# Kernel optimization log

Measured on AMD Instinct MI355X. Metric: run time of the kernel, lower is better.

The kernel has to match this reference:

```python
import jax, jax.numpy as jnp
import numpy as np

OUT = 50  # out_shape


def setup_inputs() -> dict:
    key = jax.random.key(0)
    k1, k2 = jax.random.split(key)
    B, C, H, W, N = 8, 3, 1024, 1024, 128
    x = jax.random.normal(k1, (B, C, H, W), dtype=jnp.float32)
    u = jax.random.uniform(k2, (N, 4), dtype=jnp.float32)
    # valid normalized cxcywh boxes (fully in-bounds, non-degenerate)
    cx = 0.3 + 0.4 * u[:, 0]
    cy = 0.3 + 0.4 * u[:, 1]
    w = 0.1 + 0.2 * u[:, 2]
    h = 0.1 + 0.2 * u[:, 3]
    bbox = jnp.stack([cx, cy, w, h], axis=-1)
    return {"x": x, "bbox": bbox}


def _xyxy_int(bbox, H, W):
    # its_denormalize_time: normalized cxcywh -> pixel cxcywh; its_xyxy_time: -> int xyxy
    scale = jnp.array([W, H, W, H], dtype=jnp.float32)
    b = bbox * scale
    cx, cy, w, h = b[:, 0], b[:, 1], b[:, 2], b[:, 3]
    x1 = jnp.clip(jnp.floor(cx - w / 2).astype(jnp.int32), 0, W - 1)
    y1 = jnp.clip(jnp.floor(cy - h / 2).astype(jnp.int32), 0, H - 1)
    x2 = jnp.clip(jnp.floor(cx + w / 2).astype(jnp.int32), 0, W)
    y2 = jnp.clip(jnp.floor(cy + h / 2).astype(jnp.int32), 0, H)
    x2 = jnp.maximum(x2, x1 + 1)
    y2 = jnp.maximum(y2, y1 + 1)
    return x1, y1, x2, y2


def _src_coords(lo, hi):
    # torch bilinear (align_corners=False) sampling coords inside crop [lo, hi)
    n = (hi - lo).astype(jnp.float32)
    s = jnp.clip((jnp.arange(OUT, dtype=jnp.float32) + 0.5) * n / OUT - 0.5, 0.0, n - 1.0)
    i0 = jnp.floor(s)
    w1 = s - i0
    i0 = i0.astype(jnp.int32)
    i1 = jnp.minimum(i0 + 1, hi - lo - 1)
    return lo + i0, lo + i1, w1  # absolute indices + lerp weight


def _crop_resize(x, x1, y1, x2, y2):
    # fused gather + bilinear resize for one box: [B,C,H,W] -> [B,C,OUT,OUT]
    gy0, gy1, wy = _src_coords(y1, y2)
    gx0, gx1, wx = _src_coords(x1, x2)
    v00 = x[:, :, gy0[:, None], gx0[None, :]]
    v01 = x[:, :, gy0[:, None], gx1[None, :]]
    v10 = x[:, :, gy1[:, None], gx0[None, :]]
    v11 = x[:, :, gy1[:, None], gx1[None, :]]
    top = (1.0 - wx) * v00 + wx * v01
    bot = (1.0 - wx) * v10 + wx * v11
    return (1.0 - wy)[:, None] * top + wy[:, None] * bot


def reference(x, bbox):
    B, C, H, W = x.shape
    x1, y1, x2, y2 = _xyxy_int(bbox, H, W)
    # vmap over the N boxes -> [N, B, C, OUT, OUT] (stacked version of the list)
    return jax.vmap(lambda a, b, c, d: _crop_resize(x, a, b, c, d))(x1, y1, x2, y2)
```

## Files before the change

kernel.cpp:

```cpp
#include <hip/hip_runtime.h>
#include <hip/hip_bf16.h>

#define OUTN 50
constexpr int B_ = 8, C_ = 3, H_ = 1024, W_ = 1024, N_ = 128;

__global__ __launch_bounds__(256) void crop_resize_kernel(
    const float* __restrict__ x,
    const float* __restrict__ bbox,
    float* __restrict__ out)
{
    const int blk = blockIdx.x;
    const int n  = blk / (B_ * C_);
    const int bc = blk % (B_ * C_);

    __shared__ int   sgy0[OUTN], sgy1[OUTN], sgx0[OUTN], sgx1[OUTN];
    __shared__ float swy[OUTN], swx[OUTN];

    const int t = threadIdx.x;

    if (t < 2 * OUTN) {
        const float cx = bbox[n * 4 + 0] * (float)W_;
        const float cy = bbox[n * 4 + 1] * (float)H_;
        const float bw = bbox[n * 4 + 2] * (float)W_;
        const float bh = bbox[n * 4 + 3] * (float)H_;

        int x1 = min(max((int)floorf(cx - bw / 2.0f), 0), W_ - 1);
        int y1 = min(max((int)floorf(cy - bh / 2.0f), 0), H_ - 1);
        int x2 = min(max((int)floorf(cx + bw / 2.0f), 0), W_);
        int y2 = min(max((int)floorf(cy + bh / 2.0f), 0), H_);
        x2 = max(x2, x1 + 1);
        y2 = max(y2, y1 + 1);

        const bool isY = (t >= OUTN);
        const int  i   = isY ? (t - OUTN) : t;
        const int  lo  = isY ? y1 : x1;
        const int  hi  = isY ? y2 : x2;

        const float nn = (float)(hi - lo);
        float s = ((float)i + 0.5f) * nn / 50.0f - 0.5f;
        s = fminf(fmaxf(s, 0.0f), nn - 1.0f);
        const float i0f = floorf(s);
        const float w1  = s - i0f;
        const int i0 = (int)i0f;
        const int i1 = min(i0 + 1, hi - lo - 1);

        if (isY) { sgy0[i] = lo + i0; sgy1[i] = lo + i1; swy[i] = w1; }
        else     { sgx0[i] = lo + i0; sgx1[i] = lo + i1; swx[i] = w1; }
    }
    __syncthreads();

    const float* __restrict__ xp = x + (size_t)bc * (H_ * W_);
    float* __restrict__ op = out + ((size_t)n * (B_ * C_) + bc) * (OUTN * OUTN);

    for (int idx = t; idx < OUTN * OUTN; idx += blockDim.x) {
        const int oy = idx / OUTN;
        const int ox = idx - oy * OUTN;

        const int gy0 = sgy0[oy], gy1 = sgy1[oy];
        const int gx0 = sgx0[ox], gx1 = sgx1[ox];
        const float wy = swy[oy], wx = swx[ox];

        const float v00 = xp[(size_t)gy0 * W_ + gx0];
        const float v01 = xp[(size_t)gy0 * W_ + gx1];
        const float v10 = xp[(size_t)gy1 * W_ + gx0];
        const float v11 = xp[(size_t)gy1 * W_ + gx1];

        const float top = (1.0f - wx) * v00 + wx * v01;
        const float bot = (1.0f - wx) * v10 + wx * v11;
        op[idx] = (1.0f - wy) * top + wy * bot;
    }
}

extern "C" void kernel_launch(void* const* d_in, const int* in_sizes, int n_in,
                              void* d_out, int out_size, void* d_ws, size_t ws_size,
                              hipStream_t stream) {
    const float* x    = (const float*)d_in[0];
    const float* bbox = (const float*)d_in[1];
    float* out = (float*)d_out;

    const int nblocks = N_ * B_ * C_;
    crop_resize_kernel<<<nblocks, 256, 0, stream>>>(x, bbox, out);
}
```

Measured before the change: 158.8 us.

## Remap blocks per XCD, pair bilinear taps into float2 loads, nontemporal stores

```diff
diff --git a/kernel.cpp b/kernel.cpp
--- a/kernel.cpp
+++ b/kernel.cpp
@@ -3,26 +3,32 @@
 
 #define OUTN 50
 constexpr int B_ = 8, C_ = 3, H_ = 1024, W_ = 1024, N_ = 128;
+constexpr int PLANES = B_ * C_;
+constexpr int PIX    = OUTN * OUTN;
+constexpr int TPB    = 256;
+constexpr int ITER   = (PIX + TPB - 1) / TPB;
 
-__global__ __launch_bounds__(256) void crop_resize_kernel(
+__global__ __launch_bounds__(TPB) void crop_resize_kernel(
     const float* __restrict__ x,
     const float* __restrict__ bbox,
     float* __restrict__ out)
 {
     const int blk = blockIdx.x;
-    const int n  = blk / (B_ * C_);
-    const int bc = blk % (B_ * C_);
+    const int xcd = blk & 7;
+    const int r   = blk >> 3;
+    const int bc  = xcd * 3 + (r % 3);
+    const int n   = r / 3;
 
-    __shared__ int   sgy0[OUTN], sgy1[OUTN], sgx0[OUTN], sgx1[OUTN];
-    __shared__ float swy[OUTN], swx[OUTN];
+    __shared__ int4 sy[OUTN], sx[OUTN];
 
     const int t = threadIdx.x;
 
     if (t < 2 * OUTN) {
-        const float cx = bbox[n * 4 + 0] * (float)W_;
-        const float cy = bbox[n * 4 + 1] * (float)H_;
-        const float bw = bbox[n * 4 + 2] * (float)W_;
-        const float bh = bbox[n * 4 + 3] * (float)H_;
+        const float4 bb = reinterpret_cast<const float4*>(bbox)[n];
+        const float cx = bb.x * (float)W_;
+        const float cy = bb.y * (float)H_;
+        const float bw = bb.z * (float)W_;
+        const float bh = bb.w * (float)H_;
 
         int x1 = min(max((int)floorf(cx - bw / 2.0f), 0), W_ - 1);
         int y1 = min(max((int)floorf(cy - bh / 2.0f), 0), H_ - 1);
@@ -41,33 +47,50 @@
         s = fminf(fmaxf(s, 0.0f), nn - 1.0f);
         const float i0f = floorf(s);
         const float w1  = s - i0f;
-        const int i0 = (int)i0f;
-        const int i1 = min(i0 + 1, hi - lo - 1);
+        const int   i0  = (int)i0f;
+        const int   i1  = min(i0 + 1, hi - lo - 1);
 
-        if (isY) { sgy0[i] = lo + i0; sgy1[i] = lo + i1; swy[i] = w1; }
-        else     { sgx0[i] = lo + i0; sgx1[i] = lo + i1; swx[i] = w1; }
+        if (isY) {
+            sy[i] = make_int4((lo + i0) * W_, (lo + i1) * W_,
+                              __float_as_int(w1), 0);
+        } else {
+            const int g0  = lo + i0;
+            const int a   = min(g0, W_ - 2);
+            sx[i] = make_int4(a, g0 - a, __float_as_int(w1), 0);
+        }
     }
     __syncthreads();
 
     const float* __restrict__ xp = x + (size_t)bc * (H_ * W_);
-    float* __restrict__ op = out + ((size_t)n * (B_ * C_) + bc) * (OUTN * OUTN);
+    float* __restrict__ op = out + ((size_t)n * PLANES + bc) * PIX;
 
-    for (int idx = t; idx < OUTN * OUTN; idx += blockDim.x) {
+#pragma unroll
+    for (int k = 0; k < ITER; ++k) {
+        const int idx_raw = t + k * TPB;
+        const int idx = (idx_raw < PIX) ? idx_raw : (PIX - 1);
         const int oy = idx / OUTN;
         const int ox = idx - oy * OUTN;
 
-        const int gy0 = sgy0[oy], gy1 = sgy1[oy];
-        const int gx0 = sgx0[ox], gx1 = sgx1[ox];
-        const float wy = swy[oy], wx = swx[ox];
+        const int4 yv = sy[oy];
+        const int4 xv = sx[ox];
+        const float wy = __int_as_float(yv.z);
+        const float wx = __int_as_float(xv.z);
 
-        const float v00 = xp[(size_t)gy0 * W_ + gx0];
-        const float v01 = xp[(size_t)gy0 * W_ + gx1];
-        const float v10 = xp[(size_t)gy1 * W_ + gx0];
-        const float v11 = xp[(size_t)gy1 * W_ + gx1];
+        const float2 t0 = *reinterpret_cast<const float2*>(xp + yv.x + xv.x);
+        const float2 t1 = *reinterpret_cast<const float2*>(xp + yv.y + xv.x);
+
+        const float v00 = xv.y ? t0.y : t0.x;
+        const float v01 = t0.y;
+        const float v10 = xv.y ? t1.y : t1.x;
+        const float v11 = t1.y;
 
         const float top = (1.0f - wx) * v00 + wx * v01;
         const float bot = (1.0f - wx) * v10 + wx * v11;
-        op[idx] = (1.0f - wy) * top + wy * bot;
+        const float val = (1.0f - wy) * top + wy * bot;
+
+        if (idx_raw < PIX) {
+            __builtin_nontemporal_store(val, &op[idx_raw]);
+        }
     }
 }
 
@@ -78,6 +101,5 @@
     const float* bbox = (const float*)d_in[1];
     float* out = (float*)d_out;
 
-    const int nblocks = N_ * B_ * C_;
-    crop_resize_kernel<<<nblocks, 256, 0, stream>>>(x, bbox, out);
+    crop_resize_kernel<<<N_ * PLANES, TPB, 0, stream>>>(x, bbox, out);
 }
```

After: 157.6 us. Within noise of the previous version (-0.8%).
